# Performance work log

Measured on AMD Instinct MI355X. Metric: run time of the kernel, lower is better.

Reference implementation:

```python
import jax, jax.numpy as jnp
import numpy as np

N_NODES = 50000
N_EDGES = 800000
D_IN, D_HID, D_OUT = 128, 256, 128


def _glorot(key, shape):
    fan_in, fan_out = shape[1], shape[0]
    lim = (6.0 / (fan_in + fan_out)) ** 0.5
    return jax.random.uniform(key, shape, jnp.float32, -lim, lim)


def setup_inputs() -> dict:
    key = jax.random.key(0)
    ks = jax.random.split(key, 8)
    x = jax.random.normal(ks[0], (N_NODES, D_IN), dtype=jnp.float32)
    edge_index = jax.random.randint(ks[1], (2, N_EDGES), 0, N_NODES, dtype=jnp.int64)
    # Layer 1: SAGEConv(D_IN -> D_HID); Layer 2: SAGEConv(D_HID -> D_OUT)
    # PyG SAGEConv: out = lin_l(mean_aggr(x_j)) + lin_r(x); bias lives in lin_l.
    Wl1 = _glorot(ks[2], (D_HID, D_IN))
    bl1 = jnp.zeros((D_HID,), jnp.float32)
    Wr1 = _glorot(ks[3], (D_HID, D_IN))
    Wl2 = _glorot(ks[4], (D_OUT, D_HID))
    bl2 = jnp.zeros((D_OUT,), jnp.float32)
    Wr2 = _glorot(ks[5], (D_OUT, D_HID))
    return {"x": x, "Wl1": Wl1, "bl1": bl1, "Wr1": Wr1,
            "Wl2": Wl2, "bl2": bl2, "Wr2": Wr2, "edge_index": edge_index}


def _sage_conv(x, src, dst, deg_inv, Wl, bl, Wr):
    # gather source features per edge, sum into dst buckets, normalize by in-degree
    msg_sum = jax.ops.segment_sum(x[src], dst, num_segments=N_NODES)  # [N, d_in]
    mean = msg_sum * deg_inv  # mean aggregation; isolated nodes -> zeros
    return mean @ Wl.T + bl + x @ Wr.T


def reference(x, Wl1, bl1, Wr1, Wl2, bl2, Wr2, edge_index):
    src, dst = edge_index[0], edge_index[1]
    deg = jax.ops.segment_sum(jnp.ones((N_EDGES,), jnp.float32), dst,
                              num_segments=N_NODES)
    deg_inv = (1.0 / jnp.maximum(deg, 1.0))[:, None]  # [N, 1]
    h = _sage_conv(x, src, dst, deg_inv, Wl1, bl1, Wr1)
    h = jax.nn.relu(h)  # dropout is identity in eval mode
    out = _sage_conv(h, src, dst, deg_inv, Wl2, bl2, Wr2)
    return out
```

## Files before the change

kernel.cpp:

```cpp
#include <hip/hip_runtime.h>
#include <hip/hip_fp16.h>

#define N_NODES 50000
#define N_EDGES 800000
#define D_IN 128
#define D_HID 256
#define D_OUT 128
#define NCHUNK 196
#define NTILES 3125
#define GEMM_GRID 512

typedef _Float16 f16x8 __attribute__((ext_vector_type(8)));
typedef float f32x4 __attribute__((ext_vector_type(4)));


__device__ __forceinline__ void cvt8(const float* __restrict__ src,
                                     __half* __restrict__ dstp, int i) {
    const float4* s4 = (const float4*)src;
    float4 a = s4[i * 2];
    float4 b = s4[i * 2 + 1];
    float4 o;
    __half2* op = (__half2*)&o;
    op[0] = __float22half2_rn(make_float2(a.x, a.y));
    op[1] = __float22half2_rn(make_float2(a.z, a.w));
    op[2] = __float22half2_rn(make_float2(b.x, b.y));
    op[3] = __float22half2_rn(make_float2(b.z, b.w));
    ((float4*)dstp)[i] = o;
}

__global__ __launch_bounds__(256)
void prep_kernel(const float* __restrict__ x, __half* __restrict__ xb,
                 const float* __restrict__ Wl1, const float* __restrict__ Wr1,
                 const float* __restrict__ Wl2, const float* __restrict__ Wr2,
                 __half* __restrict__ wl1h, __half* __restrict__ wr1h,
                 __half* __restrict__ wl2h, __half* __restrict__ wr2h,
                 int* __restrict__ deg) {
    int b = blockIdx.x;
    if (b < 3125) {
        int i = b * 256 + threadIdx.x;
        cvt8(x, xb, i);
    } else if (b < 3141) {
        int i = (b - 3125) * 256 + threadIdx.x;
        cvt8(Wl1, wl1h, i);
        cvt8(Wr1, wr1h, i);
        cvt8(Wl2, wl2h, i);
        cvt8(Wr2, wr2h, i);
    } else {
        int i = (b - 3141) * 256 + threadIdx.x;
        if (i < N_NODES) deg[i] = 0;
    }
}


__global__ void deg_rank_kernel(const int* __restrict__ dst, int* __restrict__ deg,
                                int* __restrict__ rank) {
    int i = blockIdx.x * blockDim.x + threadIdx.x;
    if (i < N_EDGES) rank[i] = atomicAdd(&deg[dst[i]], 1);
}

__global__ void chunk_sum(const int* __restrict__ deg, int* __restrict__ partial) {
    __shared__ int s[256];
    int i = blockIdx.x * 256 + threadIdx.x;
    s[threadIdx.x] = (i < N_NODES) ? deg[i] : 0;
    __syncthreads();
    for (int off = 128; off > 0; off >>= 1) {
        if (threadIdx.x < off) s[threadIdx.x] += s[threadIdx.x + off];
        __syncthreads();
    }
    if (threadIdx.x == 0) partial[blockIdx.x] = s[0];
}

__global__ void scatter_scan(const int* __restrict__ deg, const int* __restrict__ partial,
                             int* __restrict__ row_ptr, float* __restrict__ deg_inv) {
    __shared__ int s[256];
    __shared__ int base_s;
    const int tid = threadIdx.x;
    const int bid = blockIdx.x;
    s[tid] = (tid < bid) ? partial[tid] : 0;
    __syncthreads();
    for (int off = 128; off > 0; off >>= 1) {
        if (tid < off) s[tid] += s[tid + off];
        __syncthreads();
    }
    if (tid == 0) base_s = s[0];
    __syncthreads();
    int i = bid * 256 + tid;
    int v = (i < N_NODES) ? deg[i] : 0;
    s[tid] = v;
    __syncthreads();
    for (int off = 1; off < 256; off <<= 1) {
        int t = (tid >= off) ? s[tid - off] : 0;
        __syncthreads();
        s[tid] += t;
        __syncthreads();
    }
    if (i < N_NODES) {
        int rp = base_s + s[tid] - v;
        row_ptr[i] = rp;
        deg_inv[i] = 1.0f / fmaxf((float)v, 1.0f);
        if (i == N_NODES - 1) row_ptr[N_NODES] = N_EDGES;
    }
}

__global__ void fill_csr(const int* __restrict__ src, const int* __restrict__ dst,
                         const int* __restrict__ rank, const int* __restrict__ row_ptr,
                         int* __restrict__ csr_src) {
    int e = blockIdx.x * blockDim.x + threadIdx.x;
    if (e < N_EDGES) {
        csr_src[row_ptr[dst[e]] + rank[e]] = src[e];
    }
}


__device__ __forceinline__ void add_row(const float4& v, float2 (&acc)[4]) {
    const __half2* hp = (const __half2*)&v;
    #pragma unroll
    for (int j = 0; j < 4; ++j) {
        float2 f = __half22float2(hp[j]);
        acc[j].x += f.x;
        acc[j].y += f.y;
    }
}

template<bool ACCUM_F32>
__device__ __forceinline__ void gather_core(const __half2* __restrict__ feat,
                                            const int* __restrict__ row_ptr,
                                            const int* __restrict__ csr_src,
                                            const float* __restrict__ deg_inv,
                                            __half2* __restrict__ outh,
                                            float* __restrict__ outf) {
    const float4* feat4 = (const float4*)feat;
    const int lane = threadIdx.x & 63;
    const int g = lane >> 4;
    const int s = lane & 15;
    const int n = blockIdx.x * 4 + (threadIdx.x >> 6);
    const int beg = row_ptr[n];
    const int end = row_ptr[n + 1];
    float2 acc[4] = {};

    int idx = (beg + lane < end) ? csr_src[beg + lane] : 0;
    int base = beg;
    while (base < end) {
        int cnt = end - base;
        if (cnt > 64) cnt = 64;
        const int nbase = base + 64;
        int nidx = (nbase + lane < end) ? csr_src[nbase + lane] : 0;

        int it = 0;
        for (; it + 16 <= cnt; it += 16) {
            int s0 = __shfl(idx, it + g);
            int s1 = __shfl(idx, it + 4 + g);
            int s2 = __shfl(idx, it + 8 + g);
            int s3 = __shfl(idx, it + 12 + g);
            float4 v0 = feat4[(size_t)s0 * 16 + s];
            float4 v1 = feat4[(size_t)s1 * 16 + s];
            float4 v2 = feat4[(size_t)s2 * 16 + s];
            float4 v3 = feat4[(size_t)s3 * 16 + s];
            add_row(v0, acc);
            add_row(v1, acc);
            add_row(v2, acc);
            add_row(v3, acc);
        }
        for (; it + 4 <= cnt; it += 4) {
            int s0 = __shfl(idx, it + g);
            float4 v0 = feat4[(size_t)s0 * 16 + s];
            add_row(v0, acc);
        }
        if (it < cnt) {
            int s0 = __shfl(idx, it + g);
            if (g < cnt - it) {
                float4 v0 = feat4[(size_t)s0 * 16 + s];
                add_row(v0, acc);
            }
        }
        idx = nidx;
        base = nbase;
    }

    #pragma unroll
    for (int j = 0; j < 4; ++j) {
        acc[j].x += __shfl_xor(acc[j].x, 16);
        acc[j].y += __shfl_xor(acc[j].y, 16);
        acc[j].x += __shfl_xor(acc[j].x, 32);
        acc[j].y += __shfl_xor(acc[j].y, 32);
    }
    if (g == 0) {
        float di = deg_inv[n];
        if (ACCUM_F32) {
            float4* orow = (float4*)(outf + (size_t)n * 128);
            float4 o0 = orow[s * 2];
            float4 o1 = orow[s * 2 + 1];
            o0.x += acc[0].x * di; o0.y += acc[0].y * di;
            o0.z += acc[1].x * di; o0.w += acc[1].y * di;
            o1.x += acc[2].x * di; o1.y += acc[2].y * di;
            o1.z += acc[3].x * di; o1.w += acc[3].y * di;
            orow[s * 2] = o0;
            orow[s * 2 + 1] = o1;
        } else {
            float4 o;
            __half2* op = (__half2*)&o;
            op[0] = __float22half2_rn(make_float2(acc[0].x * di, acc[0].y * di));
            op[1] = __float22half2_rn(make_float2(acc[1].x * di, acc[1].y * di));
            op[2] = __float22half2_rn(make_float2(acc[2].x * di, acc[2].y * di));
            op[3] = __float22half2_rn(make_float2(acc[3].x * di, acc[3].y * di));
            ((float4*)(outh + (size_t)n * 64))[s] = o;
        }
    }
}

__global__ __launch_bounds__(256)
void gather_mean_h(const __half2* __restrict__ feat, const int* __restrict__ row_ptr,
                   const int* __restrict__ csr_src, const float* __restrict__ deg_inv,
                   __half2* __restrict__ outv) {
    gather_core<false>(feat, row_ptr, csr_src, deg_inv, outv, nullptr);
}

__global__ __launch_bounds__(256)
void gather_mean_add_f32(const __half2* __restrict__ feat, const int* __restrict__ row_ptr,
                         const int* __restrict__ csr_src, const float* __restrict__ deg_inv,
                         float* __restrict__ out) {
    gather_core<true>(feat, row_ptr, csr_src, deg_inv, nullptr, out);
}


#define HPAD 264

__global__ __launch_bounds__(512, 2)
void gemm_fused2(const __half* __restrict__ Aa,
                 const __half* __restrict__ Ab,
                 const __half* __restrict__ Wl1h, const __half* __restrict__ Wr1h,
                 const float* __restrict__ bias1,
                 const __half* __restrict__ B20, const __half* __restrict__ B21,
                 const float* __restrict__ bias2,
                 __half* __restrict__ P, float* __restrict__ out) {
    __shared__ __half ldsH[16][HPAD];
    const int lane = threadIdx.x & 63;
    const int wave = threadIdx.x >> 6;
    const int quad = lane >> 4;
    const int l16 = lane & 15;
    const int koff = quad * 8;

    f16x8 bf1[2][4][2];
    #pragma unroll
    for (int p = 0; p < 2; ++p) {
        const __half* __restrict__ B = p ? Wr1h : Wl1h;
        #pragma unroll
        for (int kc = 0; kc < 4; ++kc)
            #pragma unroll
            for (int nt = 0; nt < 2; ++nt)
                bf1[p][kc][nt] = *(const f16x8*)(
                    B + (size_t)(wave * 32 + nt * 16 + l16) * D_IN + kc * 32 + koff);
    }
    float bv1[2];
    #pragma unroll
    for (int nt = 0; nt < 2; ++nt) bv1[nt] = bias1[wave * 32 + nt * 16 + l16];

    f16x8 bf20[8], bf21[8];
    #pragma unroll
    for (int kc = 0; kc < 8; ++kc) {
        size_t brow = (size_t)(wave * 16 + l16) * D_HID + kc * 32 + koff;
        bf20[kc] = *(const f16x8*)(B20 + brow);
        bf21[kc] = *(const f16x8*)(B21 + brow);
    }
    float bv2 = bias2[wave * 16 + l16];

    const int g = gridDim.x;

    auto loadA = [&](int t, f16x8 (&am)[4], f16x8 (&ax)[4]) {
        const size_t arow = (size_t)(t * 16 + l16) * D_IN + koff;
        #pragma unroll
        for (int kc = 0; kc < 4; ++kc) {
            am[kc] = *(const f16x8*)(Aa + arow + kc * 32);
            ax[kc] = *(const f16x8*)(Ab + arow + kc * 32);
        }
    };

    auto step = [&](int tile, const f16x8 (&am)[4], const f16x8 (&ax)[4]) {
        f32x4 acc1[2] = {};
        #pragma unroll
        for (int kc = 0; kc < 4; ++kc)
            #pragma unroll
            for (int nt = 0; nt < 2; ++nt) {
                acc1[nt] = __builtin_amdgcn_mfma_f32_16x16x32_f16(
                    am[kc], bf1[0][kc][nt], acc1[nt], 0, 0, 0);
                acc1[nt] = __builtin_amdgcn_mfma_f32_16x16x32_f16(
                    ax[kc], bf1[1][kc][nt], acc1[nt], 0, 0, 0);
            }
        __syncthreads();
        #pragma unroll
        for (int nt = 0; nt < 2; ++nt) {
            int col = wave * 32 + nt * 16 + l16;
            #pragma unroll
            for (int r = 0; r < 4; ++r)
                ldsH[quad * 4 + r][col] =
                    __float2half(fmaxf(acc1[nt][r] + bv1[nt], 0.f));
        }
        __syncthreads();
        f32x4 acc20 = {}, acc21 = {};
        #pragma unroll
        for (int kc = 0; kc < 8; ++kc) {
            f16x8 a2 = *(const f16x8*)&ldsH[l16][kc * 32 + koff];
            acc20 = __builtin_amdgcn_mfma_f32_16x16x32_f16(a2, bf20[kc], acc20, 0, 0, 0);
            acc21 = __builtin_amdgcn_mfma_f32_16x16x32_f16(a2, bf21[kc], acc21, 0, 0, 0);
        }
        const int col = wave * 16 + l16;
        #pragma unroll
        for (int r = 0; r < 4; ++r) {
            int row = tile * 16 + quad * 4 + r;
            P[(size_t)row * D_OUT + col] = __float2half(acc20[r]);
            out[(size_t)row * D_OUT + col] = acc21[r] + bv2;
        }
    };

    f16x8 am0[4], ax0[4], am1[4], ax1[4];
    int tile = blockIdx.x;
    if (tile >= NTILES) return;
    loadA(tile, am0, ax0);
    while (true) {
        if (tile + g < NTILES) loadA(tile + g, am1, ax1);
        step(tile, am0, ax0);
        tile += g;
        if (tile >= NTILES) break;
        if (tile + g < NTILES) loadA(tile + g, am0, ax0);
        step(tile, am1, ax1);
        tile += g;
        if (tile >= NTILES) break;
    }
}

extern "C" void kernel_launch(void* const* d_in, const int* in_sizes, int n_in,
                              void* d_out, int out_size, void* d_ws, size_t ws_size,
                              hipStream_t stream) {
    const float* x   = (const float*)d_in[0];
    const float* Wl1 = (const float*)d_in[1];
    const float* bl1 = (const float*)d_in[2];
    const float* Wr1 = (const float*)d_in[3];
    const float* Wl2 = (const float*)d_in[4];
    const float* bl2 = (const float*)d_in[5];
    const float* Wr2 = (const float*)d_in[6];
    const int*   ei  = (const int*)d_in[7];
    const int* src = ei;
    const int* dst = ei + N_EDGES;
    float* out = (float*)d_out;

    char* w = (char*)d_ws;
    auto alloc = [&](size_t bytes) {
        char* r = w;
        w += (bytes + 255) & ~(size_t)255;
        return r;
    };
    int*     deg       = (int*)alloc((size_t)N_NODES * 4);
    int*     row_ptr   = (int*)alloc((size_t)(N_NODES + 1) * 4);
    int*     rank      = (int*)alloc((size_t)N_EDGES * 4);
    int*     partial   = (int*)alloc(NCHUNK * 4);
    int*     csr_src   = (int*)alloc((size_t)N_EDGES * 4);
    float*   deg_inv   = (float*)alloc((size_t)N_NODES * 4);
    __half2* xb        = (__half2*)alloc((size_t)N_NODES * 64 * 4);
    __half2* mean1     = (__half2*)alloc((size_t)N_NODES * 64 * 4);
    __half2* pb        = (__half2*)alloc((size_t)N_NODES * 64 * 4);
    __half*  wl1h      = (__half*)alloc(4 * 32768 * 2);
    __half*  wr1h = wl1h + 32768;
    __half*  wl2h = wr1h + 32768;
    __half*  wr2h = wl2h + 32768;

    prep_kernel<<<3337, 256, 0, stream>>>(x, (__half*)xb, Wl1, Wr1, Wl2, Wr2,
        wl1h, wr1h, wl2h, wr2h, deg);

    deg_rank_kernel<<<(N_EDGES + 255) / 256, 256, 0, stream>>>(dst, deg, rank);
    chunk_sum<<<NCHUNK, 256, 0, stream>>>(deg, partial);
    scatter_scan<<<NCHUNK, 256, 0, stream>>>(deg, partial, row_ptr, deg_inv);
    fill_csr<<<(N_EDGES + 255) / 256, 256, 0, stream>>>(src, dst, rank, row_ptr, csr_src);

    gather_mean_h<<<12500, 256, 0, stream>>>(xb, row_ptr, csr_src, deg_inv, mean1);

    gemm_fused2<<<GEMM_GRID, 512, 0, stream>>>(
        (const __half*)mean1, (const __half*)xb, wl1h, wr1h, bl1,
        wl2h, wr2h, bl2, (__half*)pb, out);

    gather_mean_add_f32<<<12500, 256, 0, stream>>>(pb, row_ptr, csr_src, deg_inv, out);
}
```

Before: 248.9 us.

## Split fused two-layer GEMM into separate layer kernels with global hidden buffer

Replaces the persistent fused kernel, which computed layer-1 GEMM, staged the hidden tile in LDS and ran layer-2 GEMM, with two non-persistent kernels. Each wave now handles one 16-row by 32- or 16-column output tile, and the fp16 hidden activations are written to a new global buffer. This removes the per-tile block barriers, the LDS round trip and the long register-resident weight preload, and gives more parallelism. The cost is an extra 25 MB write and read of the hidden layer, repeated loads of A rows and weights across column tiles, and one more launch.

```diff
diff --git a/kernel.cpp b/kernel.cpp
--- a/kernel.cpp
+++ b/kernel.cpp
@@ -8,7 +8,6 @@
 #define D_OUT 128
 #define NCHUNK 196
 #define NTILES 3125
-#define GEMM_GRID 512
 
 typedef _Float16 f16x8 __attribute__((ext_vector_type(8)));
 typedef float f32x4 __attribute__((ext_vector_type(4)));
@@ -223,108 +222,97 @@
 }
 
 
-#define HPAD 264
-
-__global__ __launch_bounds__(512, 2)
-void gemm_fused2(const __half* __restrict__ Aa,
-                 const __half* __restrict__ Ab,
-                 const __half* __restrict__ Wl1h, const __half* __restrict__ Wr1h,
-                 const float* __restrict__ bias1,
-                 const __half* __restrict__ B20, const __half* __restrict__ B21,
-                 const float* __restrict__ bias2,
-                 __half* __restrict__ P, float* __restrict__ out) {
-    __shared__ __half ldsH[16][HPAD];
+__global__ __launch_bounds__(256)
+void gemm_l1(const __half* __restrict__ Aa,
+             const __half* __restrict__ Ab,
+             const __half* __restrict__ Wl1h, const __half* __restrict__ Wr1h,
+             const float* __restrict__ bias1,
+             __half* __restrict__ h) {
     const int lane = threadIdx.x & 63;
-    const int wave = threadIdx.x >> 6;
+    const int task = blockIdx.x * 4 + (threadIdx.x >> 6);
+    const int rt = task >> 3;
+    const int ct = task & 7;
     const int quad = lane >> 4;
     const int l16 = lane & 15;
     const int koff = quad * 8;
 
-    f16x8 bf1[2][4][2];
-    #pragma unroll
-    for (int p = 0; p < 2; ++p) {
-        const __half* __restrict__ B = p ? Wr1h : Wl1h;
-        #pragma unroll
-        for (int kc = 0; kc < 4; ++kc)
-            #pragma unroll
-            for (int nt = 0; nt < 2; ++nt)
-                bf1[p][kc][nt] = *(const f16x8*)(
-                    B + (size_t)(wave * 32 + nt * 16 + l16) * D_IN + kc * 32 + koff);
-    }
-    float bv1[2];
-    #pragma unroll
-    for (int nt = 0; nt < 2; ++nt) bv1[nt] = bias1[wave * 32 + nt * 16 + l16];
-
-    f16x8 bf20[8], bf21[8];
-    #pragma unroll
-    for (int kc = 0; kc < 8; ++kc) {
-        size_t brow = (size_t)(wave * 16 + l16) * D_HID + kc * 32 + koff;
-        bf20[kc] = *(const f16x8*)(B20 + brow);
-        bf21[kc] = *(const f16x8*)(B21 + brow);
-    }
-    float bv2 = bias2[wave * 16 + l16];
-
-    const int g = gridDim.x;
-
-    auto loadA = [&](int t, f16x8 (&am)[4], f16x8 (&ax)[4]) {
-        const size_t arow = (size_t)(t * 16 + l16) * D_IN + koff;
-        #pragma unroll
-        for (int kc = 0; kc < 4; ++kc) {
-            am[kc] = *(const f16x8*)(Aa + arow + kc * 32);
-            ax[kc] = *(const f16x8*)(Ab + arow + kc * 32);
-        }
-    };
-
-    auto step = [&](int tile, const f16x8 (&am)[4], const f16x8 (&ax)[4]) {
-        f32x4 acc1[2] = {};
-        #pragma unroll
-        for (int kc = 0; kc < 4; ++kc)
-            #pragma unroll
-            for (int nt = 0; nt < 2; ++nt) {
-                acc1[nt] = __builtin_amdgcn_mfma_f32_16x16x32_f16(
-                    am[kc], bf1[0][kc][nt], acc1[nt], 0, 0, 0);
-                acc1[nt] = __builtin_amdgcn_mfma_f32_16x16x32_f16(
-                    ax[kc], bf1[1][kc][nt], acc1[nt], 0, 0, 0);
-            }
-        __syncthreads();
+    f16x8 am[4], ax[4];
+    const size_t arow = (size_t)(rt * 16 + l16) * D_IN + koff;
+    #pragma unroll
+    for (int kc = 0; kc < 4; ++kc) {
+        am[kc] = *(const f16x8*)(Aa + arow + kc * 32);
+        ax[kc] = *(const f16x8*)(Ab + arow + kc * 32);
+    }
+    f16x8 bl[4][2], br[4][2];
+    #pragma unroll
+    for (int kc = 0; kc < 4; ++kc)
         #pragma unroll
         for (int nt = 0; nt < 2; ++nt) {
-            int col = wave * 32 + nt * 16 + l16;
-            #pragma unroll
-            for (int r = 0; r < 4; ++r)
-                ldsH[quad * 4 + r][col] =
-                    __float2half(fmaxf(acc1[nt][r] + bv1[nt], 0.f));
-        }
-        __syncthreads();
-        f32x4 acc20 = {}, acc21 = {};
+            size_t brow = (size_t)(ct * 32 + nt * 16 + l16) * D_IN + kc * 32 + koff;
+            bl[kc][nt] = *(const f16x8*)(Wl1h + brow);
+            br[kc][nt] = *(const f16x8*)(Wr1h + brow);
+        }
+    f32x4 acc[2] = {};
+    #pragma unroll
+    for (int kc = 0; kc < 4; ++kc)
         #pragma unroll
-        for (int kc = 0; kc < 8; ++kc) {
-            f16x8 a2 = *(const f16x8*)&ldsH[l16][kc * 32 + koff];
-            acc20 = __builtin_amdgcn_mfma_f32_16x16x32_f16(a2, bf20[kc], acc20, 0, 0, 0);
-            acc21 = __builtin_amdgcn_mfma_f32_16x16x32_f16(a2, bf21[kc], acc21, 0, 0, 0);
-        }
-        const int col = wave * 16 + l16;
+        for (int nt = 0; nt < 2; ++nt) {
+            acc[nt] = __builtin_amdgcn_mfma_f32_16x16x32_f16(
+                am[kc], bl[kc][nt], acc[nt], 0, 0, 0);
+            acc[nt] = __builtin_amdgcn_mfma_f32_16x16x32_f16(
+                ax[kc], br[kc][nt], acc[nt], 0, 0, 0);
+        }
+    #pragma unroll
+    for (int nt = 0; nt < 2; ++nt) {
+        const int col = ct * 32 + nt * 16 + l16;
+        const float bv = bias1[col];
         #pragma unroll
         for (int r = 0; r < 4; ++r) {
-            int row = tile * 16 + quad * 4 + r;
-            P[(size_t)row * D_OUT + col] = __float2half(acc20[r]);
-            out[(size_t)row * D_OUT + col] = acc21[r] + bv2;
-        }
-    };
-
-    f16x8 am0[4], ax0[4], am1[4], ax1[4];
-    int tile = blockIdx.x;
-    if (tile >= NTILES) return;
-    loadA(tile, am0, ax0);
-    while (true) {
-        if (tile + g < NTILES) loadA(tile + g, am1, ax1);
-        step(tile, am0, ax0);
-        tile += g;
-        if (tile >= NTILES) break;
-        if (tile + g < NTILES) loadA(tile + g, am0, ax0);
-        step(tile, am1, ax1);
-        tile += g;
-        if (tile >= NTILES) break;
+            int row = rt * 16 + quad * 4 + r;
+            h[(size_t)row * D_HID + col] =
+                __float2half(fmaxf(acc[nt][r] + bv, 0.f));
+        }
+    }
+}
+
+__global__ __launch_bounds__(256)
+void gemm_l2(const __half* __restrict__ h,
+             const __half* __restrict__ B20, const __half* __restrict__ B21,
+             const float* __restrict__ bias2,
+             __half* __restrict__ P, float* __restrict__ out) {
+    const int lane = threadIdx.x & 63;
+    const int task = blockIdx.x * 4 + (threadIdx.x >> 6);
+    const int rt = task >> 3;
+    const int ct = task & 7;
+    const int quad = lane >> 4;
+    const int l16 = lane & 15;
+    const int koff = quad * 8;
+
+    f16x8 ah[8];
+    const size_t arow = (size_t)(rt * 16 + l16) * D_HID + koff;
+    #pragma unroll
+    for (int kc = 0; kc < 8; ++kc)
+        ah[kc] = *(const f16x8*)(h + arow + kc * 32);
+    f16x8 b0[8], b1[8];
+    #pragma unroll
+    for (int kc = 0; kc < 8; ++kc) {
+        size_t brow = (size_t)(ct * 16 + l16) * D_HID + kc * 32 + koff;
+        b0[kc] = *(const f16x8*)(B20 + brow);
+        b1[kc] = *(const f16x8*)(B21 + brow);
+    }
+    f32x4 acc0 = {}, acc1 = {};
+    #pragma unroll
+    for (int kc = 0; kc < 8; ++kc) {
+        acc0 = __builtin_amdgcn_mfma_f32_16x16x32_f16(ah[kc], b0[kc], acc0, 0, 0, 0);
+        acc1 = __builtin_amdgcn_mfma_f32_16x16x32_f16(ah[kc], b1[kc], acc1, 0, 0, 0);
+    }
+    const int col = ct * 16 + l16;
+    const float bv = bias2[col];
+    #pragma unroll
+    for (int r = 0; r < 4; ++r) {
+        int row = rt * 16 + quad * 4 + r;
+        P[(size_t)row * D_OUT + col] = __float2half(acc0[r]);
+        out[(size_t)row * D_OUT + col] = acc1[r] + bv;
     }
 }
 
@@ -357,6 +345,7 @@
     float*   deg_inv   = (float*)alloc((size_t)N_NODES * 4);
     __half2* xb        = (__half2*)alloc((size_t)N_NODES * 64 * 4);
     __half2* mean1     = (__half2*)alloc((size_t)N_NODES * 64 * 4);
+    __half*  hbuf      = (__half*)alloc((size_t)N_NODES * D_HID * 2);
     __half2* pb        = (__half2*)alloc((size_t)N_NODES * 64 * 4);
     __half*  wl1h      = (__half*)alloc(4 * 32768 * 2);
     __half*  wr1h = wl1h + 32768;
@@ -373,9 +362,10 @@
 
     gather_mean_h<<<12500, 256, 0, stream>>>(xb, row_ptr, csr_src, deg_inv, mean1);
 
-    gemm_fused2<<<GEMM_GRID, 512, 0, stream>>>(
-        (const __half*)mean1, (const __half*)xb, wl1h, wr1h, bl1,
-        wl2h, wr2h, bl2, (__half*)pb, out);
+    gemm_l1<<<6250, 256, 0, stream>>>(
+        (const __half*)mean1, (const __half*)xb, wl1h, wr1h, bl1, hbuf);
+
+    gemm_l2<<<6250, 256, 0, stream>>>(hbuf, wl2h, wr2h, bl2, (__half*)pb, out);
 
     gather_mean_add_f32<<<12500, 256, 0, stream>>>(pb, row_ptr, csr_src, deg_inv, out);
 }
```

After: 343.6 us. +38.1%, slower.
